# Kernel tuning notes

Hardware: AMD Instinct MI355X
Metric: run time of the kernel (lower is better)

The kernel has to match this reference:

```python
import jax, jax.numpy as jnp
import numpy as np

B, T, D = 2, 2048, 1024
H, DH = 16, 64


def setup_inputs() -> dict:
    key = jax.random.key(0)
    ks = jax.random.split(key, 8)
    return {
        "x": jax.random.normal(ks[0], (B, T, D), dtype=jnp.float32),
        "mask": jnp.ones((1, 1, T, T), dtype=bool),
        "Wq": jax.random.normal(ks[1], (D, D), dtype=jnp.float32) * 0.02,
        "Wk": jax.random.normal(ks[2], (D, D), dtype=jnp.float32) * 0.02,
        "Wv": jax.random.normal(ks[3], (D, D), dtype=jnp.float32) * 0.02,
        "Wo": jax.random.normal(ks[4], (D, D), dtype=jnp.float32) * 0.02,
        "S_q": jax.random.normal(ks[5], (H, DH, DH), dtype=jnp.float32),
        "S_k": jax.random.normal(ks[6], (H, DH, DH), dtype=jnp.float32),
    }


def reference(x, mask, Wq, Wk, Wv, Wo, S_q, S_k):
    b, t, _ = x.shape
    scale = DH ** (-0.5)
    # nn.Linear applies x @ W.T; our Wq etc. are the Linear weight matrices.
    def split_heads(y):
        return y.reshape(b, t, H, DH).transpose(0, 2, 1, 3)  # (B,H,T,DH)

    Q = split_heads(x @ Wq.T)
    K = split_heads(x @ Wk.T)
    V = split_heads(x @ Wv.T)
    Qp = jnp.einsum('bhtd,hde->bhte', Q, S_q)
    Kp = jnp.einsum('bhtd,hde->bhte', K, S_k)
    scores = jnp.einsum('bhte,bhse->bhts', Qp, Kp) * scale  # (B,H,T,T)
    scores = jnp.where(mask, scores, -jnp.inf)
    attn = jax.nn.softmax(scores, axis=-1)
    out = jnp.einsum('bhts,bhsd->bhtd', attn, V)
    out = out.transpose(0, 2, 1, 3).reshape(b, t, D)
    return out @ Wo.T
```

## Files before the change

### kernel.cpp

```cpp
#include <hip/hip_runtime.h>
#include <cstdint>
#include <cmath>


#define B_   2
#define T_   2048
#define Dm   1024
#define H_   16
#define DH_  64
#define Ntok (B_ * T_)
#define ND   (Ntok * Dm)
#define DD   (Dm * Dm)
#define QKS  2048

typedef _Float16 f16;
typedef _Float16 f16x4 __attribute__((ext_vector_type(4)));
typedef _Float16 f16x8 __attribute__((ext_vector_type(8)));
typedef float    f32x4 __attribute__((ext_vector_type(4)));

__device__ inline f32x4 mfma16(f16x8 a, f16x8 b, f32x4 c) {
  return __builtin_amdgcn_mfma_f32_16x16x32_f16(a, b, c, 0, 0, 0);
}

__device__ inline void async16(const void* g, void* l) {
  __builtin_amdgcn_global_load_lds(
      (const __attribute__((address_space(1))) unsigned int*)g,
      (__attribute__((address_space(3))) unsigned int*)l, 16, 0, 0);
}

__device__ inline float vmax4(f32x4 v) {
  return fmaxf(fmaxf(v[0], v[1]), fmaxf(v[2], v[3]));
}
__device__ inline float vsum4(f32x4 v) {
  return (v[0] + v[1]) + (v[2] + v[3]);
}

__global__ void cvt_f16(const float* __restrict__ X, f16* __restrict__ Y, int n) {
  int i = (blockIdx.x * 256 + threadIdx.x) * 4;
  if (i >= n) return;
  f32x4 v = *(const f32x4*)(X + i);
  f16x4 o;
#pragma unroll
  for (int j = 0; j < 4; ++j) o[j] = (f16)v[j];
  *(f16x4*)(Y + i) = o;
}

__global__ __launch_bounds__(64) void fold_w(const float* __restrict__ W,
                                             const float* __restrict__ S,
                                             f16* __restrict__ T) {
  __shared__ __align__(16) float sS[64 * 64];
  const int tid = threadIdx.x;
  const int h = blockIdx.y;
  const int d = blockIdx.x * 64 + tid;
#pragma unroll 8
  for (int i = 0; i < 64; ++i) sS[i * 64 + tid] = S[h * 4096 + i * 64 + tid];
  __syncthreads();
  float acc[64];
#pragma unroll
  for (int e = 0; e < 64; ++e) acc[e] = 0.f;
  for (int c = 0; c < 64; ++c) {
    float wv = W[(size_t)(h * 64 + c) * Dm + d];
    const f32x4* srow = (const f32x4*)&sS[c * 64];
#pragma unroll
    for (int e4 = 0; e4 < 16; ++e4) {
      f32x4 sv = srow[e4];
      acc[e4 * 4 + 0] += wv * sv[0];
      acc[e4 * 4 + 1] += wv * sv[1];
      acc[e4 * 4 + 2] += wv * sv[2];
      acc[e4 * 4 + 3] += wv * sv[3];
    }
  }
#pragma unroll
  for (int e = 0; e < 64; ++e)
    T[(size_t)(h * 64 + e) * Dm + d] = (f16)acc[e];
}

template <int OUTMODE, int TN>
__global__ __launch_bounds__(256) void gemm_bt(
    const f16* __restrict__ A, const f16* __restrict__ B,
    float* __restrict__ Cf, f16* __restrict__ Ch, f16* __restrict__ Ct,
    int M, int N, int K) {
  constexpr int AS = 128 * 32;
  constexpr int BS = TN * 32;
  constexpr int MT = (TN == 128) ? 4 : 2;
  extern __shared__ __align__(16) f16 smem[];

  const int tid = threadIdx.x;
  const int w = tid >> 6, lane = tid & 63, g = lane >> 4, ln = lane & 15;
  const int wm = (TN == 128) ? (w >> 1) * 64 : w * 32;
  const int wn = (TN == 128) ? (w & 1) * 64 : 0;
  const int bm = blockIdx.y * 128, bn = blockIdx.x * TN;

  f32x4 acc[MT][4] = {};
  const int r0 = tid >> 2;
  const int kb = (tid & 3) * 8;

  auto issue = [&](int kc, int buf) {
    f16* dA = smem + buf * AS;
    f16* dB = smem + 2 * AS + buf * BS;
#pragma unroll
    for (int i = 0; i < 2; ++i) {
      size_t aoff = (size_t)(bm + i * 64 + r0) * K + kc + kb;
      int lo = i * 4096 + w * 1024;
      async16(A + aoff, (char*)dA + lo);
      if (TN == 128 || i == 0) {
        size_t boff = (size_t)(bn + i * 64 + r0) * K + kc + kb;
        async16(B + boff, (char*)dB + lo);
      }
    }
  };

  issue(0, 0);
  const int KI = K / 32;
  for (int i = 0; i < KI; ++i) {
    __syncthreads();
    if (i + 1 < KI) issue((i + 1) * 32, (i + 1) & 1);
    const f16* cA = smem + (i & 1) * AS;
    const f16* cB = smem + 2 * AS + (i & 1) * BS;
    f16x8 af[MT];
#pragma unroll
    for (int mt = 0; mt < MT; ++mt)
      af[mt] = *(const f16x8*)&cA[(wm + mt * 16 + ln) * 32 + g * 8];
#pragma unroll
    for (int nt = 0; nt < 4; ++nt) {
      f16x8 bf = *(const f16x8*)&cB[(wn + nt * 16 + ln) * 32 + g * 8];
#pragma unroll
      for (int mt = 0; mt < MT; ++mt)
        acc[mt][nt] = mfma16(af[mt], bf, acc[mt][nt]);
    }
  }

  if (OUTMODE == 3 && bn >= 2048) {
#pragma unroll
    for (int mt = 0; mt < MT; ++mt)
#pragma unroll
      for (int nt = 0; nt < 4; ++nt) {
        int ch = bn - 2048 + wn + nt * 16 + ln;
        size_t base = (size_t)ch * Ntok + bm + wm + mt * 16 + g * 4;
        f16x4 ov;
#pragma unroll
        for (int r = 0; r < 4; ++r) ov[r] = (f16)acc[mt][nt][r];
        *(f16x4*)&Ct[base] = ov;
      }
    return;
  }
#pragma unroll
  for (int mt = 0; mt < MT; ++mt)
#pragma unroll
    for (int nt = 0; nt < 4; ++nt)
#pragma unroll
      for (int r = 0; r < 4; ++r) {
        int row = bm + wm + mt * 16 + g * 4 + r;
        int col = bn + wn + nt * 16 + ln;
        float v = acc[mt][nt][r];
        if (OUTMODE == 0) {
          Cf[(size_t)row * N + col] = v;
        } else {
          Ch[(size_t)row * QKS + col] = (f16)v;
        }
      }
}

__global__ __launch_bounds__(512) void flash_attn(
    const f16* __restrict__ QK, const f16* __restrict__ Vt,
    f16* __restrict__ O) {
  __shared__ __align__(16) f16 sKV[2][2 * 64 * 64];
  __shared__ __align__(16) f16 sP[8 * 16 * 88];
  constexpr int VOFF = 64 * 64;

  const int tid = threadIdx.x;
  const int w = tid >> 6, lane = tid & 63, g = lane >> 4, ln = lane & 15;
  const int bh = blockIdx.y, b = bh >> 4, h = bh & 15;
  const int q0 = blockIdx.x * 128 + w * 16;
  const size_t rowBase = (size_t)b * T_;
  const int hc = h * DH_;

  f16x8 qf[2];
  {
    size_t qrow = (rowBase + q0 + ln) * (size_t)QKS + hc;
#pragma unroll
    for (int s = 0; s < 2; ++s)
      qf[s] = *(const f16x8*)(QK + qrow + s * 32 + g * 8);
  }

  float mrow = -INFINITY, lrow = 0.f;
  f32x4 oacc[4] = {};

  const int srow = tid >> 3;
  const int sel = ((tid & 7) * 8) ^ ((srow & 7) * 8);
  const int ldsoff = tid * 16;

  auto issue = [&](int kc, int buf) {
    f16* base = &sKV[buf][0];
    size_t koff = (rowBase + kc + srow) * (size_t)QKS + 1024 + hc + sel;
    async16(QK + koff, (char*)base + ldsoff);
    size_t voff = (size_t)(hc + srow) * Ntok + rowBase + kc + sel;
    async16(Vt + voff, (char*)(base + VOFF) + ldsoff);
  };

  issue(0, 0);
  constexpr int NC = T_ / 64;
  for (int i = 0; i < NC; ++i) {
    __syncthreads();
    if (i + 1 < NC) issue((i + 1) * 64, (i + 1) & 1);
    const f16* cK = &sKV[i & 1][0];
    const f16* cVT = cK + VOFF;

    f32x4 s4[4];
#pragma unroll
    for (int nt = 0; nt < 4; ++nt) {
      f32x4 a = {};
#pragma unroll
      for (int s = 0; s < 2; ++s) {
        int col = (s * 32 + g * 8) ^ ((ln & 7) * 8);
        f16x8 k8 = *(const f16x8*)&cK[(nt * 16 + ln) * 64 + col];
        a = mfma16(k8, qf[s], a);
      }
      s4[nt] = a * 0.1803368801111244f;
    }

    f32x4 m4 = s4[0];
#pragma unroll
    for (int nt = 1; nt < 4; ++nt) {
      m4[0] = fmaxf(m4[0], s4[nt][0]);
      m4[1] = fmaxf(m4[1], s4[nt][1]);
      m4[2] = fmaxf(m4[2], s4[nt][2]);
      m4[3] = fmaxf(m4[3], s4[nt][3]);
    }
    float mx = vmax4(m4);
    mx = fmaxf(mx, __shfl_xor(mx, 16, 64));
    mx = fmaxf(mx, __shfl_xor(mx, 32, 64));
    float mn = fmaxf(mrow, mx);
    float alpha = __builtin_amdgcn_exp2f(mrow - mn);
    mrow = mn;
    f32x4 p4[4];
    f16x4 pk[4];
#pragma unroll
    for (int nt = 0; nt < 4; ++nt) {
#pragma unroll
      for (int r = 0; r < 4; ++r) {
        float pv = __builtin_amdgcn_exp2f(s4[nt][r] - mn);
        p4[nt][r] = pv;
        pk[nt][r] = (f16)pv;
      }
    }
    f32x4 sv4 = (p4[0] + p4[1]) + (p4[2] + p4[3]);
    float sum = vsum4(sv4);
    sum += __shfl_xor(sum, 16, 64);
    sum += __shfl_xor(sum, 32, 64);
    lrow = lrow * alpha + sum;
#pragma unroll
    for (int dt = 0; dt < 4; ++dt) oacc[dt] *= alpha;

    f16* pw = sP + w * (16 * 88);
#pragma unroll
    for (int nt = 0; nt < 4; ++nt)
      *(f16x4*)&pw[ln * 88 + nt * 16 + g * 4] = pk[nt];

    asm volatile("" ::: "memory");

#pragma unroll
    for (int s = 0; s < 2; ++s) {
      f16x8 pb = *(const f16x8*)&pw[ln * 88 + s * 32 + g * 8];
#pragma unroll
      for (int dt = 0; dt < 4; ++dt) {
        int col = (s * 32 + g * 8) ^ ((ln & 7) * 8);
        f16x8 va = *(const f16x8*)&cVT[(dt * 16 + ln) * 64 + col];
        oacc[dt] = mfma16(va, pb, oacc[dt]);
      }
    }
  }

  float rl = 1.0f / lrow;
  size_t orow = (rowBase + q0 + ln) * (size_t)Dm + hc;
#pragma unroll
  for (int dt = 0; dt < 4; ++dt) {
    f16x4 ov;
#pragma unroll
    for (int r = 0; r < 4; ++r) ov[r] = (f16)(oacc[dt][r] * rl);
    *(f16x4*)&O[orow + dt * 16 + g * 4] = ov;
  }
}

extern "C" void kernel_launch(void* const* d_in, const int* in_sizes, int n_in,
                              void* d_out, int out_size, void* d_ws, size_t ws_size,
                              hipStream_t stream) {
  const float* x  = (const float*)d_in[0];
  const float* Wq = (const float*)d_in[2];
  const float* Wk = (const float*)d_in[3];
  const float* Wv = (const float*)d_in[4];
  const float* Wo = (const float*)d_in[5];
  const float* Sq = (const float*)d_in[6];
  const float* Sk = (const float*)d_in[7];

  char* p = (char*)d_ws;
  auto alloc = [&](size_t bytes) {
    char* r = p;
    p += (bytes + 255) & ~(size_t)255;
    return r;
  };
  f16* x_f   = (f16*)alloc((size_t)ND * 2);
  f16* Wqkv  = (f16*)alloc((size_t)3 * DD * 2);
  f16* Wo_f  = (f16*)alloc((size_t)DD * 2);
  f16* QK    = (f16*)alloc((size_t)Ntok * QKS * 2);
  f16* Vt_f  = (f16*)alloc((size_t)ND * 2);
  f16* AO    = (f16*)alloc((size_t)ND * 2);

  cvt_f16<<<ND / 1024, 256, 0, stream>>>(x, x_f, ND);
  cvt_f16<<<DD / 1024, 256, 0, stream>>>(Wv, Wqkv + (size_t)2048 * Dm, DD);
  cvt_f16<<<DD / 1024, 256, 0, stream>>>(Wo, Wo_f, DD);
  fold_w<<<dim3(16, 16), 64, 0, stream>>>(Wq, Sq, Wqkv);
  fold_w<<<dim3(16, 16), 64, 0, stream>>>(Wk, Sk, Wqkv + (size_t)1024 * Dm);

  gemm_bt<3, 128><<<dim3(3072 / 128, Ntok / 128), 256, 32768, stream>>>(
      x_f, Wqkv, nullptr, QK, Vt_f, Ntok, 3072, Dm);

  flash_attn<<<dim3(T_ / 128, B_ * H_), 512, 0, stream>>>(QK, Vt_f, AO);

  gemm_bt<0, 64><<<dim3(Dm / 64, Ntok / 128), 256, 24576, stream>>>(
      AO, Wo_f, (float*)d_out, nullptr, nullptr, Ntok, Dm, Dm);
}
```

Before: 250.9 us.

## Process two query tiles per wave in flash attention and merge prep launches

The attention kernel now runs 4 waves per block instead of 8, with each wave handling 32 query rows as two 16-row tiles. Each K and V fragment read from LDS is reused across both tiles, halving LDS reads per MFMA. The output rescale is skipped when no row's max changed. Separately, the three fp32-to-fp16 conversion launches are merged into one, and the two weight-folding launches into one, to cut launch overhead. The cost is higher register pressure per wave and fewer waves available to hide latency.

```diff
diff --git a/kernel.cpp b/kernel.cpp
--- a/kernel.cpp
+++ b/kernel.cpp
@@ -35,22 +35,38 @@
   return (v[0] + v[1]) + (v[2] + v[3]);
 }
 
-__global__ void cvt_f16(const float* __restrict__ X, f16* __restrict__ Y, int n) {
+__global__ void cvt_all(const float* __restrict__ x, const float* __restrict__ Wv,
+                        const float* __restrict__ Wo, f16* __restrict__ x_f,
+                        f16* __restrict__ WvDst, f16* __restrict__ Wo_f) {
   int i = (blockIdx.x * 256 + threadIdx.x) * 4;
-  if (i >= n) return;
-  f32x4 v = *(const f32x4*)(X + i);
+  const float* src;
+  f16* dst;
+  int off;
+  if (i < ND) {
+    src = x; dst = x_f; off = i;
+  } else if (i < ND + DD) {
+    src = Wv; dst = WvDst; off = i - ND;
+  } else {
+    src = Wo; dst = Wo_f; off = i - ND - DD;
+  }
+  f32x4 v = *(const f32x4*)(src + off);
   f16x4 o;
 #pragma unroll
   for (int j = 0; j < 4; ++j) o[j] = (f16)v[j];
-  *(f16x4*)(Y + i) = o;
-}
-
-__global__ __launch_bounds__(64) void fold_w(const float* __restrict__ W,
-                                             const float* __restrict__ S,
-                                             f16* __restrict__ T) {
+  *(f16x4*)(dst + off) = o;
+}
+
+__global__ __launch_bounds__(64) void fold_w2(
+    const float* __restrict__ Wq, const float* __restrict__ Sq,
+    const float* __restrict__ Wk, const float* __restrict__ Sk,
+    f16* __restrict__ T) {
   __shared__ __align__(16) float sS[64 * 64];
   const int tid = threadIdx.x;
-  const int h = blockIdx.y;
+  const int hy = blockIdx.y;
+  const float* W = (hy < 16) ? Wq : Wk;
+  const float* S = (hy < 16) ? Sq : Sk;
+  f16* out = T + (size_t)((hy < 16) ? 0 : 1024) * Dm;
+  const int h = hy & 15;
   const int d = blockIdx.x * 64 + tid;
 #pragma unroll 8
   for (int i = 0; i < 64; ++i) sS[i * 64 + tid] = S[h * 4096 + i * 64 + tid];
@@ -72,7 +88,7 @@
   }
 #pragma unroll
   for (int e = 0; e < 64; ++e)
-    T[(size_t)(h * 64 + e) * Dm + d] = (f16)acc[e];
+    out[(size_t)(h * 64 + e) * Dm + d] = (f16)acc[e];
 }
 
 template <int OUTMODE, int TN>
@@ -161,41 +177,45 @@
       }
 }
 
-__global__ __launch_bounds__(512) void flash_attn(
+__global__ __launch_bounds__(256) void flash_attn(
     const f16* __restrict__ QK, const f16* __restrict__ Vt,
     f16* __restrict__ O) {
-  __shared__ __align__(16) f16 sKV[2][2 * 64 * 64];
-  __shared__ __align__(16) f16 sP[8 * 16 * 88];
-  constexpr int VOFF = 64 * 64;
+  __shared__ __align__(16) f16 sKV[2 * 8192];
+  __shared__ __align__(16) f16 sP[4 * 16 * 88];
+  constexpr int VOFF = 4096;
 
   const int tid = threadIdx.x;
   const int w = tid >> 6, lane = tid & 63, g = lane >> 4, ln = lane & 15;
   const int bh = blockIdx.y, b = bh >> 4, h = bh & 15;
-  const int q0 = blockIdx.x * 128 + w * 16;
+  const int q0 = blockIdx.x * 128 + w * 32;
   const size_t rowBase = (size_t)b * T_;
   const int hc = h * DH_;
 
-  f16x8 qf[2];
-  {
-    size_t qrow = (rowBase + q0 + ln) * (size_t)QKS + hc;
+  f16x8 qf[2][2];
+#pragma unroll
+  for (int t = 0; t < 2; ++t) {
+    size_t qrow = (rowBase + q0 + t * 16 + ln) * (size_t)QKS + hc;
 #pragma unroll
     for (int s = 0; s < 2; ++s)
-      qf[s] = *(const f16x8*)(QK + qrow + s * 32 + g * 8);
-  }
-
-  float mrow = -INFINITY, lrow = 0.f;
-  f32x4 oacc[4] = {};
+      qf[t][s] = *(const f16x8*)(QK + qrow + s * 32 + g * 8);
+  }
+
+  float mrow[2] = {-INFINITY, -INFINITY}, lrow[2] = {0.f, 0.f};
+  f32x4 oacc[2][4] = {};
 
   const int srow = tid >> 3;
   const int sel = ((tid & 7) * 8) ^ ((srow & 7) * 8);
-  const int ldsoff = tid * 16;
 
   auto issue = [&](int kc, int buf) {
-    f16* base = &sKV[buf][0];
-    size_t koff = (rowBase + kc + srow) * (size_t)QKS + 1024 + hc + sel;
-    async16(QK + koff, (char*)base + ldsoff);
-    size_t voff = (size_t)(hc + srow) * Ntok + rowBase + kc + sel;
-    async16(Vt + voff, (char*)(base + VOFF) + ldsoff);
+    char* base = (char*)(sKV + buf * 8192);
+#pragma unroll
+    for (int hh = 0; hh < 2; ++hh) {
+      size_t koff =
+          (rowBase + kc + hh * 32 + srow) * (size_t)QKS + 1024 + hc + sel;
+      async16(QK + koff, base + hh * 4096 + tid * 16);
+      size_t voff = (size_t)(hc + hh * 32 + srow) * Ntok + rowBase + kc + sel;
+      async16(Vt + voff, base + 8192 + hh * 4096 + tid * 16);
+    }
   };
 
   issue(0, 0);
@@ -203,82 +223,97 @@
   for (int i = 0; i < NC; ++i) {
     __syncthreads();
     if (i + 1 < NC) issue((i + 1) * 64, (i + 1) & 1);
-    const f16* cK = &sKV[i & 1][0];
+    const f16* cK = sKV + (i & 1) * 8192;
     const f16* cVT = cK + VOFF;
 
-    f32x4 s4[4];
+    const int c0 = (g * 8) ^ ((ln & 7) * 8);
+    const int c1 = (32 + g * 8) ^ ((ln & 7) * 8);
+
+    f32x4 s4[2][4];
 #pragma unroll
     for (int nt = 0; nt < 4; ++nt) {
-      f32x4 a = {};
-#pragma unroll
-      for (int s = 0; s < 2; ++s) {
-        int col = (s * 32 + g * 8) ^ ((ln & 7) * 8);
-        f16x8 k8 = *(const f16x8*)&cK[(nt * 16 + ln) * 64 + col];
-        a = mfma16(k8, qf[s], a);
-      }
-      s4[nt] = a * 0.1803368801111244f;
-    }
-
-    f32x4 m4 = s4[0];
-#pragma unroll
-    for (int nt = 1; nt < 4; ++nt) {
-      m4[0] = fmaxf(m4[0], s4[nt][0]);
-      m4[1] = fmaxf(m4[1], s4[nt][1]);
-      m4[2] = fmaxf(m4[2], s4[nt][2]);
-      m4[3] = fmaxf(m4[3], s4[nt][3]);
-    }
-    float mx = vmax4(m4);
-    mx = fmaxf(mx, __shfl_xor(mx, 16, 64));
-    mx = fmaxf(mx, __shfl_xor(mx, 32, 64));
-    float mn = fmaxf(mrow, mx);
-    float alpha = __builtin_amdgcn_exp2f(mrow - mn);
-    mrow = mn;
-    f32x4 p4[4];
-    f16x4 pk[4];
-#pragma unroll
-    for (int nt = 0; nt < 4; ++nt) {
-#pragma unroll
-      for (int r = 0; r < 4; ++r) {
-        float pv = __builtin_amdgcn_exp2f(s4[nt][r] - mn);
-        p4[nt][r] = pv;
-        pk[nt][r] = (f16)pv;
-      }
-    }
-    f32x4 sv4 = (p4[0] + p4[1]) + (p4[2] + p4[3]);
-    float sum = vsum4(sv4);
-    sum += __shfl_xor(sum, 16, 64);
-    sum += __shfl_xor(sum, 32, 64);
-    lrow = lrow * alpha + sum;
-#pragma unroll
-    for (int dt = 0; dt < 4; ++dt) oacc[dt] *= alpha;
+      int row = (nt * 16 + ln) * 64;
+      f16x8 k80 = *(const f16x8*)&cK[row + c0];
+      f16x8 k81 = *(const f16x8*)&cK[row + c1];
+#pragma unroll
+      for (int t = 0; t < 2; ++t) {
+        f32x4 a = {};
+        a = mfma16(k80, qf[t][0], a);
+        a = mfma16(k81, qf[t][1], a);
+        s4[t][nt] = a * 0.1803368801111244f;
+      }
+    }
 
     f16* pw = sP + w * (16 * 88);
-#pragma unroll
-    for (int nt = 0; nt < 4; ++nt)
-      *(f16x4*)&pw[ln * 88 + nt * 16 + g * 4] = pk[nt];
-
-    asm volatile("" ::: "memory");
+    f16x8 pb[2][2];
+#pragma unroll
+    for (int t = 0; t < 2; ++t) {
+      f32x4 m4 = s4[t][0];
+#pragma unroll
+      for (int nt = 1; nt < 4; ++nt) {
+        m4[0] = fmaxf(m4[0], s4[t][nt][0]);
+        m4[1] = fmaxf(m4[1], s4[t][nt][1]);
+        m4[2] = fmaxf(m4[2], s4[t][nt][2]);
+        m4[3] = fmaxf(m4[3], s4[t][nt][3]);
+      }
+      float mx = vmax4(m4);
+      mx = fmaxf(mx, __shfl_xor(mx, 16, 64));
+      mx = fmaxf(mx, __shfl_xor(mx, 32, 64));
+      float mn = fmaxf(mrow[t], mx);
+      float alpha = __builtin_amdgcn_exp2f(mrow[t] - mn);
+      mrow[t] = mn;
+      f32x4 p4[4];
+      f16x4 pk[4];
+#pragma unroll
+      for (int nt = 0; nt < 4; ++nt)
+#pragma unroll
+        for (int r = 0; r < 4; ++r) {
+          float pv = __builtin_amdgcn_exp2f(s4[t][nt][r] - mn);
+          p4[nt][r] = pv;
+          pk[nt][r] = (f16)pv;
+        }
+      f32x4 sv4 = (p4[0] + p4[1]) + (p4[2] + p4[3]);
+      float sum = vsum4(sv4);
+      sum += __shfl_xor(sum, 16, 64);
+      sum += __shfl_xor(sum, 32, 64);
+      lrow[t] = lrow[t] * alpha + sum;
+      if (__any(alpha != 1.0f)) {
+#pragma unroll
+        for (int dt = 0; dt < 4; ++dt) oacc[t][dt] *= alpha;
+      }
+#pragma unroll
+      for (int nt = 0; nt < 4; ++nt)
+        *(f16x4*)&pw[ln * 88 + nt * 16 + g * 4] = pk[nt];
+      asm volatile("" ::: "memory");
+#pragma unroll
+      for (int s = 0; s < 2; ++s)
+        pb[t][s] = *(const f16x8*)&pw[ln * 88 + s * 32 + g * 8];
+      asm volatile("" ::: "memory");
+    }
 
 #pragma unroll
     for (int s = 0; s < 2; ++s) {
-      f16x8 pb = *(const f16x8*)&pw[ln * 88 + s * 32 + g * 8];
+      int col = (s == 0) ? c0 : c1;
 #pragma unroll
       for (int dt = 0; dt < 4; ++dt) {
-        int col = (s * 32 + g * 8) ^ ((ln & 7) * 8);
         f16x8 va = *(const f16x8*)&cVT[(dt * 16 + ln) * 64 + col];
-        oacc[dt] = mfma16(va, pb, oacc[dt]);
-      }
-    }
-  }
-
-  float rl = 1.0f / lrow;
-  size_t orow = (rowBase + q0 + ln) * (size_t)Dm + hc;
-#pragma unroll
-  for (int dt = 0; dt < 4; ++dt) {
-    f16x4 ov;
-#pragma unroll
-    for (int r = 0; r < 4; ++r) ov[r] = (f16)(oacc[dt][r] * rl);
-    *(f16x4*)&O[orow + dt * 16 + g * 4] = ov;
+        oacc[0][dt] = mfma16(va, pb[0][s], oacc[0][dt]);
+        oacc[1][dt] = mfma16(va, pb[1][s], oacc[1][dt]);
+      }
+    }
+  }
+
+#pragma unroll
+  for (int t = 0; t < 2; ++t) {
+    float rl = 1.0f / lrow[t];
+    size_t orow = (rowBase + q0 + t * 16 + ln) * (size_t)Dm + hc;
+#pragma unroll
+    for (int dt = 0; dt < 4; ++dt) {
+      f16x4 ov;
+#pragma unroll
+      for (int r = 0; r < 4; ++r) ov[r] = (f16)(oacc[t][dt][r] * rl);
+      *(f16x4*)&O[orow + dt * 16 + g * 4] = ov;
+    }
   }
 }
 
@@ -306,16 +341,14 @@
   f16* Vt_f  = (f16*)alloc((size_t)ND * 2);
   f16* AO    = (f16*)alloc((size_t)ND * 2);
 
-  cvt_f16<<<ND / 1024, 256, 0, stream>>>(x, x_f, ND);
-  cvt_f16<<<DD / 1024, 256, 0, stream>>>(Wv, Wqkv + (size_t)2048 * Dm, DD);
-  cvt_f16<<<DD / 1024, 256, 0, stream>>>(Wo, Wo_f, DD);
-  fold_w<<<dim3(16, 16), 64, 0, stream>>>(Wq, Sq, Wqkv);
-  fold_w<<<dim3(16, 16), 64, 0, stream>>>(Wk, Sk, Wqkv + (size_t)1024 * Dm);
+  cvt_all<<<(ND + 2 * DD) / 1024, 256, 0, stream>>>(
+      x, Wv, Wo, x_f, Wqkv + (size_t)2048 * Dm, Wo_f);
+  fold_w2<<<dim3(16, 32), 64, 0, stream>>>(Wq, Sq, Wk, Sk, Wqkv);
 
   gemm_bt<3, 128><<<dim3(3072 / 128, Ntok / 128), 256, 32768, stream>>>(
       x_f, Wqkv, nullptr, QK, Vt_f, Ntok, 3072, Dm);
 
-  flash_attn<<<dim3(T_ / 128, B_ * H_), 512, 0, stream>>>(QK, Vt_f, AO);
+  flash_attn<<<dim3(T_ / 128, B_ * H_), 256, 0, stream>>>(QK, Vt_f, AO);
 
   gemm_bt<0, 64><<<dim3(Dm / 64, Ntok / 128), 256, 24576, stream>>>(
       AO, Wo_f, (float*)d_out, nullptr, nullptr, Ntok, Dm, Dm);
```

Result: faster. 238.7 us (-4.9%).
